# Performance work log

Measured on AMD Instinct MI355X. Metric: run time of the kernel, lower is better.

Reference implementation:

```python
import jax, jax.numpy as jnp
import numpy as np

EPS = 1e-5
F_BIAS = 1.0
KEEP_H = 0.7
KEEP_C = 0.7


def _block_layernorm(x, gamma, beta, n_blocks, h):
    # Normalize each of the n_blocks chunks of width h independently,
    # then apply a single per-feature gain/bias of size n_blocks*h.
    B = x.shape[0]
    xb = x.reshape(B, n_blocks, h)
    mean = jnp.mean(xb, axis=-1, keepdims=True)
    var = jnp.mean(jnp.square(xb - mean), axis=-1, keepdims=True)
    xn = (xb - mean) * jax.lax.rsqrt(var + EPS)
    return xn.reshape(B, n_blocks * h) * gamma + beta


def setup_inputs() -> dict:
    key = jax.random.key(0)
    ks = jax.random.split(key, 7)
    B, X, H = 65536, 256, 256
    x = jax.random.normal(ks[0], (B, X), dtype=jnp.float32)
    h = jax.random.normal(ks[1], (B, H), dtype=jnp.float32)
    c = jax.random.normal(ks[2], (B, H), dtype=jnp.float32)
    # orthogonal-initializer stand-in: scaled gaussian
    W_full = jax.random.normal(ks[3], (X + H, 4 * H), dtype=jnp.float32) / np.sqrt(X + H)
    bias = jnp.zeros((4 * H,), dtype=jnp.float32)
    g1 = jnp.ones((4 * H,), dtype=jnp.float32)
    b1 = jnp.zeros((4 * H,), dtype=jnp.float32)
    g2 = jnp.ones((H,), dtype=jnp.float32)
    b2 = jnp.zeros((H,), dtype=jnp.float32)
    mask_h = jax.random.uniform(ks[4], (B, H), dtype=jnp.float32)
    mask_c = jax.random.uniform(ks[5], (B, H), dtype=jnp.float32)
    return {"x": x, "h": h, "c": c, "W_full": W_full, "bias": bias,
            "g1": g1, "b1": b1, "g2": g2, "b2": b2,
            "mask_h": mask_h, "mask_c": mask_c}


def reference(x, h, c, W_full, bias, g1, b1, g2, b2, mask_h, mask_c):
    H = h.shape[1]
    concat = jnp.concatenate([x, h], axis=1) @ W_full + bias       # [B, 4H]
    concat = _block_layernorm(concat, g1, b1, 4, H)
    i, j, f, o = jnp.split(concat, 4, axis=1)
    new_c = c * jax.nn.sigmoid(f + F_BIAS) + jax.nn.sigmoid(i) * jnp.tanh(j)
    new_c = _block_layernorm(new_c, g2, b2, 1, H)
    new_h = jnp.tanh(new_c) * jax.nn.sigmoid(o)
    # zoneout: keep the NEW state with prob keep, else carry over old state
    mh = (mask_h < KEEP_H).astype(new_h.dtype)
    mc = (mask_c < KEEP_C).astype(new_c.dtype)
    new_h = mh * new_h + (1.0 - mh) * h
    new_c = mc * new_c + (1.0 - mc) * c
    return (new_h, new_c)
```

## Files before the change

kernel.cpp:

```cpp
#include <hip/hip_runtime.h>


#define NTHREADS 512
#define TILE_M 64
#define PRE_STRIDE 20

typedef _Float16 half8 __attribute__((ext_vector_type(8)));
typedef _Float16 half4v __attribute__((ext_vector_type(4)));
typedef float float4v __attribute__((ext_vector_type(4)));

__device__ __forceinline__ void async16(const void* g, void* l) {
  __builtin_amdgcn_global_load_lds(
      (const __attribute__((address_space(1))) unsigned int*)g,
      (__attribute__((address_space(3))) unsigned int*)l, 16, 0, 0);
}

__device__ __forceinline__ float sigm(float x) {
  return __fdividef(1.0f, 1.0f + __expf(-x));
}
__device__ __forceinline__ float tanh_fast(float x) {
  return 2.0f * __fdividef(1.0f, 1.0f + __expf(-2.0f * x)) - 1.0f;
}

__global__ __launch_bounds__(256) void wt_kernel(const float* __restrict__ W,
                                                 _Float16* __restrict__ Wt) {
  __shared__ float tile[64][65];
  const int bn = blockIdx.x << 6;
  const int bk = blockIdx.y << 6;
  const int tid = threadIdx.x;
#pragma unroll
  for (int i = 0; i < 16; ++i) {
    int idx = (i << 8) + tid;
    int kk = idx >> 6, nn = idx & 63;
    tile[kk][nn] = W[(size_t)(bk + kk) * 1024 + bn + nn];
  }
  __syncthreads();
#pragma unroll
  for (int i = 0; i < 16; ++i) {
    int idx = (i << 8) + tid;
    int nn = idx >> 6, kk = idx & 63;
    Wt[(size_t)(bn + nn) * 512 + bk + kk] = (_Float16)tile[kk][nn];
  }
}

__global__ __launch_bounds__(NTHREADS, 2) void lstm_fused(
    const float* __restrict__ x, const float* __restrict__ hin,
    const float* __restrict__ cin, const _Float16* __restrict__ Wt,
    const float* __restrict__ bias, const float* __restrict__ g1,
    const float* __restrict__ b1, const float* __restrict__ g2,
    const float* __restrict__ b2, const float* __restrict__ mhp,
    const float* __restrict__ mcp, float* __restrict__ out) {
  extern __shared__ char smem[];
  _Float16* aT = (_Float16*)smem;
  _Float16* wTh = (_Float16*)(smem + 4096);
  _Float16* preT = (_Float16*)smem;

  const int tid = threadIdx.x;
  const int wave = tid >> 6;
  const int lane = tid & 63;
  const int l15 = lane & 15;
  const int quad = lane >> 4;
  const int blockRow = blockIdx.x * TILE_M;

  float4v acc[4][8];
#pragma unroll
  for (int s = 0; s < 4; ++s)
#pragma unroll
    for (int c = 0; c < 8; ++c) acc[s][c] = (float4v){0.f, 0.f, 0.f, 0.f};

  const int arow = tid >> 3;
  const int ap4 = (tid & 7) << 2;
  const float* xrow = x + (size_t)(blockRow + arow) * 256 + ap4;
  const float* hrow = hin + (size_t)(blockRow + arow) * 256 + ap4;
  _Float16* adst = aT + arow * 32 + (((ap4 >> 3) ^ (arow & 3)) << 3) + (ap4 & 4);

  const int wnl0 = tid >> 2;
  const int wj = (tid & 3) ^ (wnl0 & 3);
  const char* wg = (const char*)Wt + (size_t)wnl0 * 1024 + wj * 16;
  char* wl = (char*)wTh + tid * 16;

  const int aslot = quad ^ (l15 & 3);

  for (int iter = 0; iter < 16; ++iter) {
    {
      const float* src = (iter < 8) ? (xrow + iter * 32) : (hrow + (iter - 8) * 32);
      float4 v = *(const float4*)src;
      half4v hv = {(_Float16)v.x, (_Float16)v.y, (_Float16)v.z, (_Float16)v.w};
      *(half4v*)adst = hv;
    }
#pragma unroll
    for (int it = 0; it < 4; ++it)
      async16(wg + it * 131072 + iter * 64, wl + it * 8192);
    __syncthreads();

    half8 af[4];
#pragma unroll
    for (int s = 0; s < 4; ++s)
      af[s] = *(const half8*)(aT + (s * 16 + l15) * 32 + aslot * 8);
    {
      half8 bf[4];
#pragma unroll
      for (int cc = 0; cc < 4; ++cc) {
        int nl = wave * 64 + cc * 16 + l15;
        bf[cc] = *(const half8*)(wTh + nl * 32 + aslot * 8);
      }
#pragma unroll
      for (int s = 0; s < 4; ++s)
#pragma unroll
        for (int cc = 0; cc < 4; ++cc)
          acc[s][cc] = __builtin_amdgcn_mfma_f32_16x16x32_f16(af[s], bf[cc], acc[s][cc], 0, 0, 0);
    }
    __syncthreads();
#pragma unroll
    for (int it = 0; it < 4; ++it)
      async16(wg + 524288 + it * 131072 + iter * 64, wl + it * 8192);
    __syncthreads();
    {
      half8 bf[4];
#pragma unroll
      for (int cc = 0; cc < 4; ++cc) {
        int nl = wave * 64 + cc * 16 + l15;
        bf[cc] = *(const half8*)(wTh + nl * 32 + aslot * 8);
      }
#pragma unroll
      for (int s = 0; s < 4; ++s)
#pragma unroll
        for (int cc = 0; cc < 4; ++cc)
          acc[s][4 + cc] =
              __builtin_amdgcn_mfma_f32_16x16x32_f16(af[s], bf[cc], acc[s][4 + cc], 0, 0, 0);
    }
    __syncthreads();
  }

  float* out_h = out;
  float* out_c = out + (size_t)65536 * 256;
  const int er = tid >> 5;
  const int et = tid & 31;

#pragma unroll
  for (int p = 0; p < 4; ++p) {
    __syncthreads();
#pragma unroll
    for (int c = 0; c < 8; ++c) {
      int n = ((c >> 2) << 9) + wave * 64 + ((c & 3) << 4) + l15;
      float4v a = acc[p][c];
      half4v hv = {(_Float16)a.x, (_Float16)a.y, (_Float16)a.z, (_Float16)a.w};
      *(half4v*)(preT + n * PRE_STRIDE + (quad << 2)) = hv;
    }
    __syncthreads();

    const int rg = blockRow + (p << 4) + er;
    float mean1[4], rstd1[4];
#pragma unroll
    for (int ch = 0; ch < 4; ++ch) {
      float s = 0.f, q = 0.f;
#pragma unroll
      for (int ss = 0; ss < 8; ++ss) {
        int n = (ch << 8) + (ss << 5) + et;
        float v = (float)preT[n * PRE_STRIDE + er] + bias[n];
        s += v;
        q += v * v;
      }
#pragma unroll
      for (int m = 1; m < 32; m <<= 1) {
        s += __shfl_xor(s, m, 32);
        q += __shfl_xor(q, m, 32);
      }
      float mu = s * (1.0f / 256.0f);
      mean1[ch] = mu;
      rstd1[ch] = __frsqrt_rn(q * (1.0f / 256.0f) - mu * mu + 1e-5f);
    }

    float ncp[8], so[8], cv[8];
    float s2 = 0.f, q2 = 0.f;
#pragma unroll
    for (int ss = 0; ss < 8; ++ss) {
      int hc = (ss << 5) + et;
      float iv = ((float)preT[(hc)*PRE_STRIDE + er] + bias[hc] - mean1[0]) * rstd1[0] * g1[hc] + b1[hc];
      float jv = ((float)preT[(256 + hc) * PRE_STRIDE + er] + bias[256 + hc] - mean1[1]) * rstd1[1] * g1[256 + hc] + b1[256 + hc];
      float fv = ((float)preT[(512 + hc) * PRE_STRIDE + er] + bias[512 + hc] - mean1[2]) * rstd1[2] * g1[512 + hc] + b1[512 + hc];
      float ov = ((float)preT[(768 + hc) * PRE_STRIDE + er] + bias[768 + hc] - mean1[3]) * rstd1[3] * g1[768 + hc] + b1[768 + hc];
      float cval = cin[(size_t)rg * 256 + hc];
      float nc = cval * sigm(fv + 1.0f) + sigm(iv) * tanh_fast(jv);
      ncp[ss] = nc;
      so[ss] = sigm(ov);
      cv[ss] = cval;
      s2 += nc;
      q2 += nc * nc;
    }
#pragma unroll
    for (int m = 1; m < 32; m <<= 1) {
      s2 += __shfl_xor(s2, m, 32);
      q2 += __shfl_xor(q2, m, 32);
    }
    float mu2 = s2 * (1.0f / 256.0f);
    float rstd2 = __frsqrt_rn(q2 * (1.0f / 256.0f) - mu2 * mu2 + 1e-5f);
#pragma unroll
    for (int ss = 0; ss < 8; ++ss) {
      int hc = (ss << 5) + et;
      size_t gi = (size_t)rg * 256 + hc;
      float ncn = (ncp[ss] - mu2) * rstd2 * g2[hc] + b2[hc];
      float nh = tanh_fast(ncn) * so[ss];
      float hval = hin[gi];
      out_h[gi] = (mhp[gi] < 0.7f) ? nh : hval;
      out_c[gi] = (mcp[gi] < 0.7f) ? ncn : cv[ss];
    }
  }
}

extern "C" void kernel_launch(void* const* d_in, const int* in_sizes, int n_in,
                              void* d_out, int out_size, void* d_ws, size_t ws_size,
                              hipStream_t stream) {
  (void)in_sizes; (void)n_in; (void)out_size; (void)ws_size;
  const float* x = (const float*)d_in[0];
  const float* h = (const float*)d_in[1];
  const float* c = (const float*)d_in[2];
  const float* W = (const float*)d_in[3];
  const float* bias = (const float*)d_in[4];
  const float* g1 = (const float*)d_in[5];
  const float* b1 = (const float*)d_in[6];
  const float* g2 = (const float*)d_in[7];
  const float* b2 = (const float*)d_in[8];
  const float* mh = (const float*)d_in[9];
  const float* mc = (const float*)d_in[10];
  _Float16* Wt = (_Float16*)d_ws;

  wt_kernel<<<dim3(16, 8), dim3(256), 0, stream>>>(W, Wt);
  lstm_fused<<<dim3(1024), dim3(NTHREADS), 40960, stream>>>(
      x, h, c, Wt, bias, g1, b1, g2, b2, mh, mc, (float*)d_out);
}
```

Baseline: 510.2 us.

## Double-buffer weight tiles in LDS and prefetch activations across iterations

Adds a second LDS buffer for the weight half-tiles so the next half's async global-to-LDS loads are issued while MFMAs run on the current half. The next x/h chunk is loaded into registers early and written to LDS at the end of the iteration. This cuts barriers per K-step from four to two. It also changes the XOR swizzle pattern and raises MFMA issue priority with s_setprio. In exchange, LDS per block grows to about 68 KB, which tightens occupancy headroom.

```diff
diff --git a/kernel.cpp b/kernel.cpp
--- a/kernel.cpp
+++ b/kernel.cpp
@@ -51,8 +51,9 @@
     const float* __restrict__ b2, const float* __restrict__ mhp,
     const float* __restrict__ mcp, float* __restrict__ out) {
   extern __shared__ char smem[];
-  _Float16* aT = (_Float16*)smem;
-  _Float16* wTh = (_Float16*)(smem + 4096);
+  _Float16* abuf = (_Float16*)smem;
+  _Float16* wbuf0 = (_Float16*)(smem + 4096);
+  _Float16* wbuf1 = (_Float16*)(smem + 36864);
   _Float16* preT = (_Float16*)smem;
 
   const int tid = threadIdx.x;
@@ -72,62 +73,76 @@
   const int ap4 = (tid & 7) << 2;
   const float* xrow = x + (size_t)(blockRow + arow) * 256 + ap4;
   const float* hrow = hin + (size_t)(blockRow + arow) * 256 + ap4;
-  _Float16* adst = aT + arow * 32 + (((ap4 >> 3) ^ (arow & 3)) << 3) + (ap4 & 4);
+  const int aswz = (arow ^ (arow >> 2)) & 3;
+  _Float16* adst = abuf + arow * 32 + (((ap4 >> 3) ^ aswz) << 3) + (ap4 & 4);
 
   const int wnl0 = tid >> 2;
-  const int wj = (tid & 3) ^ (wnl0 & 3);
+  const int wj = (tid & 3) ^ ((wnl0 ^ (wnl0 >> 2)) & 3);
   const char* wg = (const char*)Wt + (size_t)wnl0 * 1024 + wj * 16;
-  char* wl = (char*)wTh + tid * 16;
-
-  const int aslot = quad ^ (l15 & 3);
-
-  for (int iter = 0; iter < 16; ++iter) {
-    {
-      const float* src = (iter < 8) ? (xrow + iter * 32) : (hrow + (iter - 8) * 32);
-      float4 v = *(const float4*)src;
-      half4v hv = {(_Float16)v.x, (_Float16)v.y, (_Float16)v.z, (_Float16)v.w};
-      *(half4v*)adst = hv;
-    }
+  char* wl0 = (char*)wbuf0 + tid * 16;
+  char* wl1 = (char*)wbuf1 + tid * 16;
+
+  const int aslot = quad ^ ((l15 ^ (l15 >> 2)) & 3);
+
+  {
+    float4 v = *(const float4*)xrow;
+    half4v hv = {(_Float16)v.x, (_Float16)v.y, (_Float16)v.z, (_Float16)v.w};
+    *(half4v*)adst = hv;
+  }
+#pragma unroll
+  for (int it = 0; it < 4; ++it) async16(wg + it * 131072, wl0 + it * 8192);
+  __syncthreads();
+
+  float4 av;
+  for (int i = 0; i < 16; ++i) {
 #pragma unroll
     for (int it = 0; it < 4; ++it)
-      async16(wg + it * 131072 + iter * 64, wl + it * 8192);
-    __syncthreads();
-
+      async16(wg + 524288 + it * 131072 + i * 64, wl1 + it * 8192);
+    if (i < 15) {
+      const float* s1 = (i + 1 < 8) ? (xrow + (i + 1) * 32) : (hrow + (i - 7) * 32);
+      av = *(const float4*)s1;
+    }
     half8 af[4];
 #pragma unroll
     for (int s = 0; s < 4; ++s)
-      af[s] = *(const half8*)(aT + (s * 16 + l15) * 32 + aslot * 8);
+      af[s] = *(const half8*)(abuf + (s * 16 + l15) * 32 + aslot * 8);
     {
       half8 bf[4];
 #pragma unroll
-      for (int cc = 0; cc < 4; ++cc) {
-        int nl = wave * 64 + cc * 16 + l15;
-        bf[cc] = *(const half8*)(wTh + nl * 32 + aslot * 8);
-      }
+      for (int cc = 0; cc < 4; ++cc)
+        bf[cc] = *(const half8*)(wbuf0 + (wave * 64 + cc * 16 + l15) * 32 + aslot * 8);
+      __builtin_amdgcn_s_setprio(1);
 #pragma unroll
       for (int s = 0; s < 4; ++s)
 #pragma unroll
         for (int cc = 0; cc < 4; ++cc)
           acc[s][cc] = __builtin_amdgcn_mfma_f32_16x16x32_f16(af[s], bf[cc], acc[s][cc], 0, 0, 0);
-    }
-    __syncthreads();
-#pragma unroll
-    for (int it = 0; it < 4; ++it)
-      async16(wg + 524288 + it * 131072 + iter * 64, wl + it * 8192);
-    __syncthreads();
+      __builtin_amdgcn_s_setprio(0);
+    }
+    __syncthreads();
+
+    if (i < 15) {
+#pragma unroll
+      for (int it = 0; it < 4; ++it)
+        async16(wg + it * 131072 + (i + 1) * 64, wl0 + it * 8192);
+    }
     {
       half8 bf[4];
 #pragma unroll
-      for (int cc = 0; cc < 4; ++cc) {
-        int nl = wave * 64 + cc * 16 + l15;
-        bf[cc] = *(const half8*)(wTh + nl * 32 + aslot * 8);
-      }
+      for (int cc = 0; cc < 4; ++cc)
+        bf[cc] = *(const half8*)(wbuf1 + (wave * 64 + cc * 16 + l15) * 32 + aslot * 8);
+      __builtin_amdgcn_s_setprio(1);
 #pragma unroll
       for (int s = 0; s < 4; ++s)
 #pragma unroll
         for (int cc = 0; cc < 4; ++cc)
           acc[s][4 + cc] =
               __builtin_amdgcn_mfma_f32_16x16x32_f16(af[s], bf[cc], acc[s][4 + cc], 0, 0, 0);
+      __builtin_amdgcn_s_setprio(0);
+    }
+    if (i < 15) {
+      half4v hv = {(_Float16)av.x, (_Float16)av.y, (_Float16)av.z, (_Float16)av.w};
+      *(half4v*)adst = hv;
     }
     __syncthreads();
   }
@@ -226,6 +241,6 @@
   _Float16* Wt = (_Float16*)d_ws;
 
   wt_kernel<<<dim3(16, 8), dim3(256), 0, stream>>>(W, Wt);
-  lstm_fused<<<dim3(1024), dim3(NTHREADS), 40960, stream>>>(
+  lstm_fused<<<dim3(1024), dim3(NTHREADS), 69632, stream>>>(
       x, h, c, Wt, bias, g1, b1, g2, b2, mh, mc, (float*)d_out);
 }
```

New measurement: 480.6 us. -5.8%, faster.
